# Kernel optimization log

Hardware: AMD Instinct MI355X
Metric: run time of the kernel (lower is better)

## Reference

```python
import jax, jax.numpy as jnp
import numpy as np
import math

B, S, D, H, DK = 2, 4096, 512, 8, 64

def setup_inputs() -> dict:
    key = jax.random.key(0)
    ks = jax.random.split(key, 11)
    scale = 1.0 / math.sqrt(D)
    inp = {
        'q': jax.random.normal(ks[0], (B, S, D), jnp.float32),
        'k': jax.random.normal(ks[1], (B, S, D), jnp.float32),
        'v': jax.random.normal(ks[2], (B, S, D), jnp.float32),
        # causal mask: True = masked (as consumed by masked_fill)
        'mask': jnp.triu(jnp.ones((S, S), jnp.bool_), k=1)[None, None, :, :],
        'wq': jax.random.normal(ks[3], (D, D), jnp.float32) * scale,
        'bq': jnp.zeros((D,), jnp.float32),
        'wk': jax.random.normal(ks[4], (D, D), jnp.float32) * scale,
        'bk': jnp.zeros((D,), jnp.float32),
        'wv': jax.random.normal(ks[5], (D, D), jnp.float32) * scale,
        'bv': jnp.zeros((D,), jnp.float32),
        'wo': jax.random.normal(ks[6], (D, D), jnp.float32) * scale,
        'bo': jnp.zeros((D,), jnp.float32),
    }
    return inp

def reference(q, k, v, mask, wq, bq, wk, bk, wv, bv, wo, bo):
    # torch nn.Linear: y = x @ W^T + b
    def proj(x, w, b):
        return x @ w.T + b
    def heads(x):  # [B,S,D] -> [B,H,S,DK]
        return x.reshape(B, S, H, DK).transpose(0, 2, 1, 3)
    qh = heads(proj(q, wq, bq))
    kh = heads(proj(k, wk, bk))
    vh = heads(proj(v, wv, bv))
    scores = jnp.einsum('bhqd,bhkd->bhqk', qh, kh) / math.sqrt(DK)
    # NOTE: faithful to source, masked positions are filled with -1e-09 (not -inf)
    scores = jnp.where(mask, jnp.float32(-1e-09), scores)
    attn = jax.nn.softmax(scores, axis=-1)
    x = jnp.einsum('bhqk,bhkd->bhqd', attn, vh)
    x = x.transpose(0, 2, 1, 3).reshape(B, S, D)
    return proj(x, wo, bo)
```

## Files before the change

kernel.cpp:

```cpp
#include <hip/hip_runtime.h>
#include <math.h>

#define SS 4096
#define DD 512
#define HH 8
#define DKK 64

#define MSUB 4.0f
#define W_MASK 0.0183156393f

typedef _Float16 half8_t __attribute__((ext_vector_type(8)));
typedef _Float16 half4_t __attribute__((ext_vector_type(4)));
typedef float f32x4 __attribute__((ext_vector_type(4)));
typedef float f32x16 __attribute__((ext_vector_type(16)));

__device__ __forceinline__ f32x4 mfma16(half8_t a, half8_t b, f32x4 c) {
    return __builtin_amdgcn_mfma_f32_16x16x32_f16(a, b, c, 0, 0, 0);
}
__device__ __forceinline__ f32x16 mfma32(half8_t a, half8_t b, f32x16 c) {
    return __builtin_amdgcn_mfma_f32_32x32x16_f16(a, b, c, 0, 0, 0);
}
__device__ __forceinline__ f32x16 zero16() {
    f32x16 z;
#pragma unroll
    for (int i = 0; i < 16; i++) z[i] = 0.f;
    return z;
}
__device__ __forceinline__ void gld_lds16(const _Float16* g, _Float16* l) {
    __builtin_amdgcn_global_load_lds((const __attribute__((address_space(1))) void*)g,
                                     (__attribute__((address_space(3))) void*)l, 16, 0, 0);
}

__global__ __launch_bounds__(256) void cvt_prep(
    const float* __restrict__ q, const float* __restrict__ k, const float* __restrict__ v,
    const float* __restrict__ wq, const float* __restrict__ wk,
    const float* __restrict__ wv, const float* __restrict__ wo,
    _Float16* qf, _Float16* kf, _Float16* vf,
    _Float16* wqf, _Float16* wkf, _Float16* wvf, _Float16* wof)
{
    const float* srcs[7] = {q, k, v, wq, wk, wv, wo};
    _Float16* dsts[7] = {qf, kf, vf, wqf, wkf, wvf, wof};
    const int ns[7] = {4194304, 4194304, 4194304, 262144, 262144, 262144, 262144};
    int t = blockIdx.y;
    size_t i0 = ((size_t)blockIdx.x * 256 + threadIdx.x) * 8;
    if (i0 >= (size_t)ns[t]) return;
    const float* s = srcs[t];
    _Float16* d = dsts[t];
    float4 a = *(const float4*)(s + i0);
    float4 b = *(const float4*)(s + i0 + 4);
    half8_t h = {(_Float16)a.x, (_Float16)a.y, (_Float16)a.z, (_Float16)a.w,
                 (_Float16)b.x, (_Float16)b.y, (_Float16)b.z, (_Float16)b.w};
    *(half8_t*)(d + i0) = h;
}

__global__ __launch_bounds__(256, 3) void gemm_qkv(
    const _Float16* __restrict__ qf, const _Float16* __restrict__ kf,
    const _Float16* __restrict__ vf,
    const _Float16* __restrict__ wqf, const _Float16* __restrict__ wkf,
    const _Float16* __restrict__ wvf,
    const float* __restrict__ bq, const float* __restrict__ bk,
    const float* __restrict__ bv,
    _Float16* __restrict__ Qf, _Float16* __restrict__ Kf,
    _Float16* __restrict__ Vf, _Float16* __restrict__ Vt)
{
    __shared__ __align__(16) _Float16 Al[128][72];
    __shared__ __align__(16) _Float16 Wl[128][72];
    const int z = blockIdx.z;
    const _Float16* A = z == 0 ? qf : (z == 1 ? kf : vf);
    const _Float16* W = z == 0 ? wqf : (z == 1 ? wkf : wvf);
    const float* bias = z == 0 ? bq : (z == 1 ? bk : bv);

    const int tid = threadIdx.x;
    const int w = tid >> 6, lane = tid & 63, q = lane >> 4, cc = lane & 15;
    const int mtile = blockIdx.x * 128, ntile = blockIdx.y * 128;
    const int mw = (w & 1) * 64, nw = (w >> 1) * 64;

    f32x4 acc[4][4];
#pragma unroll
    for (int i = 0; i < 4; i++)
#pragma unroll
        for (int j = 0; j < 4; j++) {
            f32x4 zf = {0.f, 0.f, 0.f, 0.f};
            acc[i][j] = zf;
        }

    for (int kt = 0; kt < 512; kt += 64) {
        __syncthreads();
#pragma unroll
        for (int i = 0; i < 4; i++) {
            int idx = i * 256 + tid;
            int row = idx >> 3, c8 = (idx & 7) * 8;
            *(float4*)(&Al[row][c8]) =
                *(const float4*)(A + (size_t)(mtile + row) * 512 + kt + c8);
            *(float4*)(&Wl[row][c8]) =
                *(const float4*)(W + (size_t)(ntile + row) * 512 + kt + c8);
        }
        __syncthreads();
#pragma unroll
        for (int kh = 0; kh < 2; kh++) {
            half8_t ar[4], br[4];
#pragma unroll
            for (int i = 0; i < 4; i++)
                ar[i] = *(const half8_t*)(&Al[mw + i * 16 + cc][kh * 32 + q * 8]);
#pragma unroll
            for (int j = 0; j < 4; j++)
                br[j] = *(const half8_t*)(&Wl[nw + j * 16 + cc][kh * 32 + q * 8]);
#pragma unroll
            for (int i = 0; i < 4; i++)
#pragma unroll
                for (int j = 0; j < 4; j++)
                    acc[i][j] = mfma16(ar[i], br[j], acc[i][j]);
        }
    }

#pragma unroll
    for (int jb = 0; jb < 4; jb++) {
        int n = ntile + nw + jb * 16 + cc;
        float bvv = bias[n];
        int h = n >> 6, dkl = n & 63;
#pragma unroll
        for (int it = 0; it < 4; it++) {
            int m0 = mtile + mw + it * 16 + q * 4;
            int b = m0 >> 12;
            int sq0 = m0 & 4095;
            int bh = b * 8 + h;
            if (z == 0) {
#pragma unroll
                for (int r = 0; r < 4; r++) {
                    int sq = sq0 + r;
                    size_t addr = ((size_t)(bh * 128 + (sq >> 5)) * 4 + (dkl >> 4)) * 512
                                  + ((sq & 31) + 32 * ((dkl >> 3) & 1)) * 8 + (dkl & 7);
                    Qf[addr] = (_Float16)(acc[it][jb][r] + bvv);
                }
            } else if (z == 1) {
#pragma unroll
                for (int r = 0; r < 4; r++) {
                    int sq = sq0 + r;
                    size_t addr = ((size_t)(bh * 64 + (sq >> 6)) * 8
                                   + ((sq >> 5) & 1) * 4 + (dkl >> 4)) * 512
                                  + ((sq & 31) + 32 * ((dkl >> 3) & 1)) * 8 + (dkl & 7);
                    Kf[addr] = (_Float16)(acc[it][jb][r] + bvv);
                }
            } else {
                half4_t pk;
#pragma unroll
                for (int r = 0; r < 4; r++) {
                    int sq = sq0 + r;
                    float val = acc[it][jb][r] + bvv;
                    pk[r] = (_Float16)val;
                    size_t addr = ((size_t)(bh * 64 + (sq >> 6)) * 8
                                   + ((sq >> 4) & 3) * 2 + (dkl >> 5)) * 512
                                  + ((dkl & 31) + 32 * ((sq >> 2) & 1)) * 8
                                  + ((sq & 3) + 4 * ((sq >> 3) & 1));
                    Vf[addr] = (_Float16)val;
                }
                *(half4_t*)(Vt + ((size_t)bh * 64 + dkl) * SS + sq0) = pk;
            }
        }
    }
}

__global__ __launch_bounds__(256) void suffix_v(const _Float16* __restrict__ Vt,
                                                _Float16* __restrict__ SufVt)
{
    __shared__ float csum[4][65];
    const int bh = blockIdx.x >> 4;
    const int dk = (blockIdx.x & 15) * 4 + (threadIdx.x >> 6);
    const int dki = threadIdx.x >> 6;
    const int c = threadIdx.x & 63;
    const _Float16* vp = Vt + ((size_t)bh * 64 + dk) * SS + c * 64;

    half8_t v8[8];
    float acc = 0.f;
#pragma unroll
    for (int j = 0; j < 8; j++) {
        v8[j] = *(const half8_t*)(vp + j * 8);
#pragma unroll
        for (int t = 0; t < 8; t++) acc += (float)v8[j][t];
    }
    csum[dki][c] = acc;
    __syncthreads();
    if (threadIdx.x < 4) {
        float a = 0.f;
        for (int c2 = 63; c2 >= 0; c2--) {
            float t2 = csum[threadIdx.x][c2];
            csum[threadIdx.x][c2] = a;
            a += t2;
        }
    }
    __syncthreads();
    float a = csum[dki][c];
    _Float16* op = SufVt + ((size_t)bh * 64 + dk) * SS + c * 64;
#pragma unroll
    for (int j = 7; j >= 0; j--) {
        half8_t o8;
#pragma unroll
        for (int t = 7; t >= 0; t--) {
            o8[t] = (_Float16)a;
            a += (float)v8[j][t];
        }
        *(half8_t*)(op + j * 8) = o8;
    }
}

__global__ __launch_bounds__(256, 3) void attn_kernel(
    const _Float16* __restrict__ Qf, const _Float16* __restrict__ Kf,
    const _Float16* __restrict__ Vf, const _Float16* __restrict__ SufVt,
    _Float16* __restrict__ X)
{
    __shared__ __align__(16) _Float16 lds[8192];
    const int tid = threadIdx.x;
    const int w = tid >> 6, lane = tid & 63;
    const int h5 = lane >> 5, l31 = lane & 31;
    const int bh = blockIdx.x & 15;
    const int g = blockIdx.x >> 4;
    const int qt = (g < 16) ? (31 - g) : (g - 16);
    const int qbase = qt * 128 + w * 32;
    const int jdiag = qbase & ~63;
    const int jsd = (qbase >> 5) & 1;
    const int jmaxb = qt * 128 + 64;

    const _Float16* qp = Qf + (size_t)(bh * 128 + (qbase >> 5)) * 4 * 512 + lane * 8;
    half8_t qfr[4];
#pragma unroll
    for (int s = 0; s < 4; s++) qfr[s] = *(const half8_t*)(qp + s * 512);

    const _Float16* Kb = Kf + (size_t)bh * 64 * 4096;
    const _Float16* Vb = Vf + (size_t)bh * 64 * 4096;

    f32x16 o0 = zero16(), o1 = zero16();
    float lsum = 0.f;

    for (int j0 = 0; j0 <= jmaxb; j0 += 64) {
        __syncthreads();
        {
            const int jblk = j0 >> 6;
            const _Float16* kg = Kb + (size_t)jblk * 4096 + (w * 2) * 512 + lane * 8;
            const _Float16* vg = Vb + (size_t)jblk * 4096 + (w * 2) * 512 + lane * 8;
            gld_lds16(kg,       &lds[(w * 2) * 512]);
            gld_lds16(kg + 512, &lds[(w * 2 + 1) * 512]);
            gld_lds16(vg,       &lds[4096 + (w * 2) * 512]);
            gld_lds16(vg + 512, &lds[4096 + (w * 2 + 1) * 512]);
        }
        __syncthreads();
        if (j0 > jdiag) continue;
        const bool diag = (j0 == jdiag);
        const bool do1 = (!diag) || (jsd == 1);

        f32x16 sa = zero16(), sb = zero16();
#pragma unroll
        for (int s = 0; s < 4; s++)
            sa = mfma32(*(const half8_t*)(&lds[s * 512 + lane * 8]), qfr[s], sa);
        if (do1) {
#pragma unroll
            for (int s = 0; s < 4; s++)
                sb = mfma32(*(const half8_t*)(&lds[(4 + s) * 512 + lane * 8]), qfr[s], sb);
        }

        half8_t p0a, p0b, p1a, p1b;
        const int mg = qbase + l31;
        const bool mask0 = diag && (jsd == 0);
        const bool mask1 = diag && (jsd == 1);
#pragma unroll
        for (int i = 0; i < 16; i++) {
            float p = __expf(fmaf(sa[i], 0.125f, -MSUB));
            if (mask0) {
                int jg = j0 + (i & 3) + 8 * (i >> 2) + 4 * h5;
                if (jg > mg) p = 0.f;
            }
            lsum += p;
            if (i < 8) p0a[i] = (_Float16)p; else p0b[i - 8] = (_Float16)p;
        }
        if (do1) {
#pragma unroll
            for (int i = 0; i < 16; i++) {
                float p = __expf(fmaf(sb[i], 0.125f, -MSUB));
                if (mask1) {
                    int jg = j0 + 32 + (i & 3) + 8 * (i >> 2) + 4 * h5;
                    if (jg > mg) p = 0.f;
                }
                lsum += p;
                if (i < 8) p1a[i] = (_Float16)p; else p1b[i - 8] = (_Float16)p;
            }
        }

        o0 = mfma32(p0a, *(const half8_t*)(&lds[4096 + 0 * 512 + lane * 8]), o0);
        o1 = mfma32(p0a, *(const half8_t*)(&lds[4096 + 1 * 512 + lane * 8]), o1);
        o0 = mfma32(p0b, *(const half8_t*)(&lds[4096 + 2 * 512 + lane * 8]), o0);
        o1 = mfma32(p0b, *(const half8_t*)(&lds[4096 + 3 * 512 + lane * 8]), o1);
        if (do1) {
            o0 = mfma32(p1a, *(const half8_t*)(&lds[4096 + 4 * 512 + lane * 8]), o0);
            o1 = mfma32(p1a, *(const half8_t*)(&lds[4096 + 5 * 512 + lane * 8]), o1);
            o0 = mfma32(p1b, *(const half8_t*)(&lds[4096 + 6 * 512 + lane * 8]), o0);
            o1 = mfma32(p1b, *(const half8_t*)(&lds[4096 + 7 * 512 + lane * 8]), o1);
        }
    }

    lsum += __shfl_xor(lsum, 32);

    const int b = bh >> 3, hh = bh & 7;
#pragma unroll
    for (int r = 0; r < 16; r++) {
        int ml = (r & 3) + 8 * (r >> 2) + 4 * h5;
        float lv = __shfl(lsum, ml);
        int s = qbase + ml;
        float iv = 1.f / (lv + (float)(SS - 1 - s) * W_MASK);
        float sv0 = (float)SufVt[((size_t)bh * 64 + l31) * SS + s];
        float sv1 = (float)SufVt[((size_t)bh * 64 + 32 + l31) * SS + s];
        X[((size_t)b * SS + s) * DD + hh * 64 + l31] =
            (_Float16)((o0[r] + W_MASK * sv0) * iv);
        X[((size_t)b * SS + s) * DD + hh * 64 + 32 + l31] =
            (_Float16)((o1[r] + W_MASK * sv1) * iv);
    }
}

__global__ __launch_bounds__(256, 4) void gemm_out(
    const _Float16* __restrict__ A, const _Float16* __restrict__ W,
    const float* __restrict__ bias, float* __restrict__ Cout)
{
    __shared__ __align__(16) _Float16 Al[128][72];
    __shared__ __align__(16) _Float16 Wl[64][72];
    const int tid = threadIdx.x;
    const int w = tid >> 6, lane = tid & 63, q = lane >> 4, cc = lane & 15;
    const int mtile = blockIdx.x * 128, ntile = blockIdx.y * 64;
    const int mw = (w & 1) * 64, nw = (w >> 1) * 32;

    f32x4 acc[4][2];
#pragma unroll
    for (int i = 0; i < 4; i++)
#pragma unroll
        for (int j = 0; j < 2; j++) {
            f32x4 zf = {0.f, 0.f, 0.f, 0.f};
            acc[i][j] = zf;
        }

    for (int kt = 0; kt < 512; kt += 64) {
        __syncthreads();
#pragma unroll
        for (int i = 0; i < 4; i++) {
            int idx = i * 256 + tid;
            int row = idx >> 3, c8 = (idx & 7) * 8;
            *(float4*)(&Al[row][c8]) =
                *(const float4*)(A + (size_t)(mtile + row) * 512 + kt + c8);
        }
#pragma unroll
        for (int i = 0; i < 2; i++) {
            int idx = i * 256 + tid;
            int row = idx >> 3, c8 = (idx & 7) * 8;
            *(float4*)(&Wl[row][c8]) =
                *(const float4*)(W + (size_t)(ntile + row) * 512 + kt + c8);
        }
        __syncthreads();
#pragma unroll
        for (int kh = 0; kh < 2; kh++) {
            half8_t ar[4], br[2];
#pragma unroll
            for (int i = 0; i < 4; i++)
                ar[i] = *(const half8_t*)(&Al[mw + i * 16 + cc][kh * 32 + q * 8]);
#pragma unroll
            for (int j = 0; j < 2; j++)
                br[j] = *(const half8_t*)(&Wl[nw + j * 16 + cc][kh * 32 + q * 8]);
#pragma unroll
            for (int i = 0; i < 4; i++)
#pragma unroll
                for (int j = 0; j < 2; j++)
                    acc[i][j] = mfma16(ar[i], br[j], acc[i][j]);
        }
    }

#pragma unroll
    for (int j = 0; j < 2; j++) {
        int coln = ntile + nw + j * 16 + cc;
        float bvv = bias[coln];
#pragma unroll
        for (int i = 0; i < 4; i++) {
            int m0 = mtile + mw + i * 16 + q * 4;
#pragma unroll
            for (int r = 0; r < 4; r++)
                Cout[(size_t)(m0 + r) * 512 + coln] = acc[i][j][r] + bvv;
        }
    }
}

extern "C" void kernel_launch(void* const* d_in, const int* in_sizes, int n_in,
                              void* d_out, int out_size, void* d_ws, size_t ws_size,
                              hipStream_t stream) {
    const float* q  = (const float*)d_in[0];
    const float* k  = (const float*)d_in[1];
    const float* v  = (const float*)d_in[2];
    const float* wq = (const float*)d_in[4];
    const float* bq = (const float*)d_in[5];
    const float* wk = (const float*)d_in[6];
    const float* bk = (const float*)d_in[7];
    const float* wv = (const float*)d_in[8];
    const float* bv = (const float*)d_in[9];
    const float* wo = (const float*)d_in[10];
    const float* bo = (const float*)d_in[11];
    float* out = (float*)d_out;

    char* ws = (char*)d_ws;
    const size_t MB = (size_t)1024 * 1024;
    _Float16* qf  = (_Float16*)(ws);
    _Float16* kf  = (_Float16*)(ws + 8 * MB);
    _Float16* vf  = (_Float16*)(ws + 16 * MB);
    _Float16* wqf = (_Float16*)(ws + 24 * MB);
    _Float16* wkf = (_Float16*)(ws + 24 * MB + 512 * 1024);
    _Float16* wvf = (_Float16*)(ws + 25 * MB);
    _Float16* wof = (_Float16*)(ws + 25 * MB + 512 * 1024);
    _Float16* Qfr = (_Float16*)(ws + 26 * MB);
    _Float16* Kfr = (_Float16*)(ws + 34 * MB);
    _Float16* Vfr = (_Float16*)(ws + 42 * MB);
    _Float16* Vt  = (_Float16*)(ws + 50 * MB);
    _Float16* SufVt = qf;
    _Float16* Xa    = kf;

    hipLaunchKernelGGL(cvt_prep, dim3(2048, 7), dim3(256), 0, stream,
                       q, k, v, wq, wk, wv, wo, qf, kf, vf, wqf, wkf, wvf, wof);
    hipLaunchKernelGGL(gemm_qkv, dim3(64, 4, 3), dim3(256), 0, stream,
                       qf, kf, vf, wqf, wkf, wvf, bq, bk, bv, Qfr, Kfr, Vfr, Vt);
    hipLaunchKernelGGL(suffix_v, dim3(256), dim3(256), 0, stream, Vt, SufVt);
    hipLaunchKernelGGL(attn_kernel, dim3(512), dim3(256), 0, stream,
                       Qfr, Kfr, Vfr, SufVt, Xa);
    hipLaunchKernelGGL(gemm_out, dim3(64, 8), dim3(256), 0, stream, Xa, wof, bo, out);
}
```

Before: 288.4 us.

## Drop LDS staging in attention, pair waves for causal balance, use direct-to-LDS loads in GEMMs

The attention kernel no longer stages K/V tiles in shared memory behind block-wide barriers. Each wave reads its MFMA operands straight from global memory in the pre-swizzled layout. Waves are paired so each block holds one short and one long causal row range, replacing the old per-block tile ordering, and the diagonal block is split out so full blocks skip mask checks. The two GEMMs swap register-staged LDS copies for direct global-to-LDS loads into an unpadded layout, which risks LDS bank conflicts and relies on L2/cache reuse for K/V in attention.

```diff
diff --git a/kernel.cpp b/kernel.cpp
--- a/kernel.cpp
+++ b/kernel.cpp
@@ -63,8 +63,7 @@
     _Float16* __restrict__ Qf, _Float16* __restrict__ Kf,
     _Float16* __restrict__ Vf, _Float16* __restrict__ Vt)
 {
-    __shared__ __align__(16) _Float16 Al[128][72];
-    __shared__ __align__(16) _Float16 Wl[128][72];
+    __shared__ __align__(16) _Float16 smem[16384];
     const int z = blockIdx.z;
     const _Float16* A = z == 0 ? qf : (z == 1 ? kf : vf);
     const _Float16* W = z == 0 ? wqf : (z == 1 ? wkf : wvf);
@@ -74,6 +73,7 @@
     const int w = tid >> 6, lane = tid & 63, q = lane >> 4, cc = lane & 15;
     const int mtile = blockIdx.x * 128, ntile = blockIdx.y * 128;
     const int mw = (w & 1) * 64, nw = (w >> 1) * 64;
+    const int srow = lane >> 3, scol = (lane & 7) * 8;
 
     f32x4 acc[4][4];
 #pragma unroll
@@ -88,12 +88,9 @@
         __syncthreads();
 #pragma unroll
         for (int i = 0; i < 4; i++) {
-            int idx = i * 256 + tid;
-            int row = idx >> 3, c8 = (idx & 7) * 8;
-            *(float4*)(&Al[row][c8]) =
-                *(const float4*)(A + (size_t)(mtile + row) * 512 + kt + c8);
-            *(float4*)(&Wl[row][c8]) =
-                *(const float4*)(W + (size_t)(ntile + row) * 512 + kt + c8);
+            int r0 = w * 32 + i * 8;
+            gld_lds16(A + (size_t)(mtile + r0 + srow) * 512 + kt + scol, &smem[r0 * 64]);
+            gld_lds16(W + (size_t)(ntile + r0 + srow) * 512 + kt + scol, &smem[8192 + r0 * 64]);
         }
         __syncthreads();
 #pragma unroll
@@ -101,10 +98,10 @@
             half8_t ar[4], br[4];
 #pragma unroll
             for (int i = 0; i < 4; i++)
-                ar[i] = *(const half8_t*)(&Al[mw + i * 16 + cc][kh * 32 + q * 8]);
+                ar[i] = *(const half8_t*)(&smem[(mw + i * 16 + cc) * 64 + kh * 32 + q * 8]);
 #pragma unroll
             for (int j = 0; j < 4; j++)
-                br[j] = *(const half8_t*)(&Wl[nw + j * 16 + cc][kh * 32 + q * 8]);
+                br[j] = *(const half8_t*)(&smem[8192 + (nw + j * 16 + cc) * 64 + kh * 32 + q * 8]);
 #pragma unroll
             for (int i = 0; i < 4; i++)
 #pragma unroll
@@ -203,96 +200,105 @@
     }
 }
 
-__global__ __launch_bounds__(256, 3) void attn_kernel(
+__device__ __forceinline__ void exp_pack(const f32x16& s, half8_t& pa, half8_t& pb,
+                                         float& lsum) {
+#pragma unroll
+    for (int i = 0; i < 16; i++) {
+        float p = __expf(fmaf(s[i], 0.125f, -MSUB));
+        lsum += p;
+        if (i < 8) pa[i] = (_Float16)p; else pb[i - 8] = (_Float16)p;
+    }
+}
+__device__ __forceinline__ void exp_pack_mask(const f32x16& s, int j0, int mg, int h5,
+                                              half8_t& pa, half8_t& pb, float& lsum) {
+#pragma unroll
+    for (int i = 0; i < 16; i++) {
+        int jg = j0 + (i & 3) + 8 * (i >> 2) + 4 * h5;
+        float p = __expf(fmaf(s[i], 0.125f, -MSUB));
+        if (jg > mg) p = 0.f;
+        lsum += p;
+        if (i < 8) pa[i] = (_Float16)p; else pb[i - 8] = (_Float16)p;
+    }
+}
+
+__global__ __launch_bounds__(256, 2) void attn_kernel(
     const _Float16* __restrict__ Qf, const _Float16* __restrict__ Kf,
     const _Float16* __restrict__ Vf, const _Float16* __restrict__ SufVt,
     _Float16* __restrict__ X)
 {
-    __shared__ __align__(16) _Float16 lds[8192];
     const int tid = threadIdx.x;
     const int w = tid >> 6, lane = tid & 63;
     const int h5 = lane >> 5, l31 = lane & 31;
     const int bh = blockIdx.x & 15;
-    const int g = blockIdx.x >> 4;
-    const int qt = (g < 16) ? (31 - g) : (g - 16);
-    const int qbase = qt * 128 + w * 32;
+    const int seg = blockIdx.x >> 4;
+    const int wp = w >> 1;
+    const int qg = ((w & 1) == 0) ? (seg * 2 + wp) : (127 - seg * 2 - wp);
+
+    const int qbase = qg * 32;
     const int jdiag = qbase & ~63;
     const int jsd = (qbase >> 5) & 1;
-    const int jmaxb = qt * 128 + 64;
+    const int mg = qbase + l31;
 
     const _Float16* qp = Qf + (size_t)(bh * 128 + (qbase >> 5)) * 4 * 512 + lane * 8;
     half8_t qfr[4];
 #pragma unroll
     for (int s = 0; s < 4; s++) qfr[s] = *(const half8_t*)(qp + s * 512);
 
-    const _Float16* Kb = Kf + (size_t)bh * 64 * 4096;
-    const _Float16* Vb = Vf + (size_t)bh * 64 * 4096;
+    const _Float16* Kb = Kf + (size_t)bh * 64 * 4096 + lane * 8;
+    const _Float16* Vb = Vf + (size_t)bh * 64 * 4096 + lane * 8;
 
     f32x16 o0 = zero16(), o1 = zero16();
     float lsum = 0.f;
 
-    for (int j0 = 0; j0 <= jmaxb; j0 += 64) {
-        __syncthreads();
-        {
-            const int jblk = j0 >> 6;
-            const _Float16* kg = Kb + (size_t)jblk * 4096 + (w * 2) * 512 + lane * 8;
-            const _Float16* vg = Vb + (size_t)jblk * 4096 + (w * 2) * 512 + lane * 8;
-            gld_lds16(kg,       &lds[(w * 2) * 512]);
-            gld_lds16(kg + 512, &lds[(w * 2 + 1) * 512]);
-            gld_lds16(vg,       &lds[4096 + (w * 2) * 512]);
-            gld_lds16(vg + 512, &lds[4096 + (w * 2 + 1) * 512]);
-        }
-        __syncthreads();
-        if (j0 > jdiag) continue;
-        const bool diag = (j0 == jdiag);
-        const bool do1 = (!diag) || (jsd == 1);
-
+    const int nfull = jdiag >> 6;
+    for (int jblk = 0; jblk < nfull; jblk++) {
+        const _Float16* kg = Kb + (size_t)jblk * 4096;
+        const _Float16* vg = Vb + (size_t)jblk * 4096;
         f32x16 sa = zero16(), sb = zero16();
 #pragma unroll
         for (int s = 0; s < 4; s++)
-            sa = mfma32(*(const half8_t*)(&lds[s * 512 + lane * 8]), qfr[s], sa);
-        if (do1) {
+            sa = mfma32(*(const half8_t*)(kg + s * 512), qfr[s], sa);
+#pragma unroll
+        for (int s = 0; s < 4; s++)
+            sb = mfma32(*(const half8_t*)(kg + (4 + s) * 512), qfr[s], sb);
+        half8_t p0a, p0b, p1a, p1b;
+        exp_pack(sa, p0a, p0b, lsum);
+        exp_pack(sb, p1a, p1b, lsum);
+        o0 = mfma32(p0a, *(const half8_t*)(vg + 0 * 512), o0);
+        o1 = mfma32(p0a, *(const half8_t*)(vg + 1 * 512), o1);
+        o0 = mfma32(p0b, *(const half8_t*)(vg + 2 * 512), o0);
+        o1 = mfma32(p0b, *(const half8_t*)(vg + 3 * 512), o1);
+        o0 = mfma32(p1a, *(const half8_t*)(vg + 4 * 512), o0);
+        o1 = mfma32(p1a, *(const half8_t*)(vg + 5 * 512), o1);
+        o0 = mfma32(p1b, *(const half8_t*)(vg + 6 * 512), o0);
+        o1 = mfma32(p1b, *(const half8_t*)(vg + 7 * 512), o1);
+    }
+
+    {
+        const _Float16* kg = Kb + (size_t)nfull * 4096;
+        const _Float16* vg = Vb + (size_t)nfull * 4096;
+        f32x16 sa = zero16();
+#pragma unroll
+        for (int s = 0; s < 4; s++)
+            sa = mfma32(*(const half8_t*)(kg + s * 512), qfr[s], sa);
+        half8_t p0a, p0b;
+        if (jsd == 0) exp_pack_mask(sa, jdiag, mg, h5, p0a, p0b, lsum);
+        else          exp_pack(sa, p0a, p0b, lsum);
+        o0 = mfma32(p0a, *(const half8_t*)(vg + 0 * 512), o0);
+        o1 = mfma32(p0a, *(const half8_t*)(vg + 1 * 512), o1);
+        o0 = mfma32(p0b, *(const half8_t*)(vg + 2 * 512), o0);
+        o1 = mfma32(p0b, *(const half8_t*)(vg + 3 * 512), o1);
+        if (jsd == 1) {
+            f32x16 sb = zero16();
 #pragma unroll
             for (int s = 0; s < 4; s++)
-                sb = mfma32(*(const half8_t*)(&lds[(4 + s) * 512 + lane * 8]), qfr[s], sb);
-        }
-
-        half8_t p0a, p0b, p1a, p1b;
-        const int mg = qbase + l31;
-        const bool mask0 = diag && (jsd == 0);
-        const bool mask1 = diag && (jsd == 1);
-#pragma unroll
-        for (int i = 0; i < 16; i++) {
-            float p = __expf(fmaf(sa[i], 0.125f, -MSUB));
-            if (mask0) {
-                int jg = j0 + (i & 3) + 8 * (i >> 2) + 4 * h5;
-                if (jg > mg) p = 0.f;
-            }
-            lsum += p;
-            if (i < 8) p0a[i] = (_Float16)p; else p0b[i - 8] = (_Float16)p;
-        }
-        if (do1) {
-#pragma unroll
-            for (int i = 0; i < 16; i++) {
-                float p = __expf(fmaf(sb[i], 0.125f, -MSUB));
-                if (mask1) {
-                    int jg = j0 + 32 + (i & 3) + 8 * (i >> 2) + 4 * h5;
-                    if (jg > mg) p = 0.f;
-                }
-                lsum += p;
-                if (i < 8) p1a[i] = (_Float16)p; else p1b[i - 8] = (_Float16)p;
-            }
-        }
-
-        o0 = mfma32(p0a, *(const half8_t*)(&lds[4096 + 0 * 512 + lane * 8]), o0);
-        o1 = mfma32(p0a, *(const half8_t*)(&lds[4096 + 1 * 512 + lane * 8]), o1);
-        o0 = mfma32(p0b, *(const half8_t*)(&lds[4096 + 2 * 512 + lane * 8]), o0);
-        o1 = mfma32(p0b, *(const half8_t*)(&lds[4096 + 3 * 512 + lane * 8]), o1);
-        if (do1) {
-            o0 = mfma32(p1a, *(const half8_t*)(&lds[4096 + 4 * 512 + lane * 8]), o0);
-            o1 = mfma32(p1a, *(const half8_t*)(&lds[4096 + 5 * 512 + lane * 8]), o1);
-            o0 = mfma32(p1b, *(const half8_t*)(&lds[4096 + 6 * 512 + lane * 8]), o0);
-            o1 = mfma32(p1b, *(const half8_t*)(&lds[4096 + 7 * 512 + lane * 8]), o1);
+                sb = mfma32(*(const half8_t*)(kg + (4 + s) * 512), qfr[s], sb);
+            half8_t p1a, p1b;
+            exp_pack_mask(sb, jdiag + 32, mg, h5, p1a, p1b, lsum);
+            o0 = mfma32(p1a, *(const half8_t*)(vg + 4 * 512), o0);
+            o1 = mfma32(p1a, *(const half8_t*)(vg + 5 * 512), o1);
+            o0 = mfma32(p1b, *(const half8_t*)(vg + 6 * 512), o0);
+            o1 = mfma32(p1b, *(const half8_t*)(vg + 7 * 512), o1);
         }
     }
 
@@ -318,12 +324,12 @@
     const _Float16* __restrict__ A, const _Float16* __restrict__ W,
     const float* __restrict__ bias, float* __restrict__ Cout)
 {
-    __shared__ __align__(16) _Float16 Al[128][72];
-    __shared__ __align__(16) _Float16 Wl[64][72];
+    __shared__ __align__(16) _Float16 smem[12288];
     const int tid = threadIdx.x;
     const int w = tid >> 6, lane = tid & 63, q = lane >> 4, cc = lane & 15;
     const int mtile = blockIdx.x * 128, ntile = blockIdx.y * 64;
     const int mw = (w & 1) * 64, nw = (w >> 1) * 32;
+    const int srow = lane >> 3, scol = (lane & 7) * 8;
 
     f32x4 acc[4][2];
 #pragma unroll
@@ -338,17 +344,13 @@
         __syncthreads();
 #pragma unroll
         for (int i = 0; i < 4; i++) {
-            int idx = i * 256 + tid;
-            int row = idx >> 3, c8 = (idx & 7) * 8;
-            *(float4*)(&Al[row][c8]) =
-                *(const float4*)(A + (size_t)(mtile + row) * 512 + kt + c8);
+            int r0 = w * 32 + i * 8;
+            gld_lds16(A + (size_t)(mtile + r0 + srow) * 512 + kt + scol, &smem[r0 * 64]);
         }
 #pragma unroll
         for (int i = 0; i < 2; i++) {
-            int idx = i * 256 + tid;
-            int row = idx >> 3, c8 = (idx & 7) * 8;
-            *(float4*)(&Wl[row][c8]) =
-                *(const float4*)(W + (size_t)(ntile + row) * 512 + kt + c8);
+            int r0 = w * 16 + i * 8;
+            gld_lds16(W + (size_t)(ntile + r0 + srow) * 512 + kt + scol, &smem[8192 + r0 * 64]);
         }
         __syncthreads();
 #pragma unroll
@@ -356,10 +358,10 @@
             half8_t ar[4], br[2];
 #pragma unroll
             for (int i = 0; i < 4; i++)
-                ar[i] = *(const half8_t*)(&Al[mw + i * 16 + cc][kh * 32 + q * 8]);
+                ar[i] = *(const half8_t*)(&smem[(mw + i * 16 + cc) * 64 + kh * 32 + q * 8]);
 #pragma unroll
             for (int j = 0; j < 2; j++)
-                br[j] = *(const half8_t*)(&Wl[nw + j * 16 + cc][kh * 32 + q * 8]);
+                br[j] = *(const half8_t*)(&smem[8192 + (nw + j * 16 + cc) * 64 + kh * 32 + q * 8]);
 #pragma unroll
             for (int i = 0; i < 4; i++)
 #pragma unroll
```

Measured after the change: 265.1 us. 1.09x faster.
